# Optimization experiments

Measured on AMD Instinct MI355X. Metric: run time of the kernel, lower is better.

Reference implementation:

```python
import jax, jax.numpy as jnp
import numpy as np

B, C, H, W = 8, 256, 128, 128
HEADS = 4
HEAD_DIM = C // HEADS  # 64
SCALE = HEAD_DIM ** -0.5


def setup_inputs() -> dict:
    key = jax.random.key(0)
    k1, k2, k3 = jax.random.split(key, 3)
    x = jax.random.normal(k1, (B, C, H, W), dtype=jnp.float32)
    # 1x1 convs == per-pixel linear layers; kaiming-ish small init
    Wqkv = jax.random.normal(k2, (3 * C, C), dtype=jnp.float32) * (1.0 / np.sqrt(C))
    bqkv = jnp.zeros((3 * C,), dtype=jnp.float32)
    Wproj = jax.random.normal(k3, (C, C), dtype=jnp.float32) * (1.0 / np.sqrt(C))
    bproj = jnp.zeros((C,), dtype=jnp.float32)
    return {"x": x, "Wqkv": Wqkv, "bqkv": bqkv, "Wproj": Wproj, "bproj": bproj}


def reference(x, Wqkv, bqkv, Wproj, bproj):
    b, c, h, w = x.shape
    hw = h * w
    xf = x.reshape(b, c, hw)  # [b, c, hw]
    # 1x1 conv QKV projection
    qkv = jnp.einsum('bcn,oc->bon', xf, Wqkv) + bqkv[None, :, None]  # [b, 3c, hw]
    qkv = qkv.reshape(b, 3, HEADS, HEAD_DIM, hw)
    q, k, v = qkv[:, 0], qkv[:, 1], qkv[:, 2]  # each [b, heads, d, hw]
    # channel attention: [b, heads, d, d]
    attn = jnp.einsum('bhdn,bhen->bhde', q, k) * SCALE
    attn = jax.nn.softmax(attn, axis=-1)
    out = jnp.einsum('bhde,bhen->bhdn', attn, v).reshape(b, c, hw)
    # output 1x1 conv
    out = jnp.einsum('bcn,oc->bon', out, Wproj) + bproj[None, :, None]
    return out.reshape(b, c, h, w)
```

## Files before the change

kernel.cpp:

```cpp
#include <hip/hip_runtime.h>
#include <hip/hip_bf16.h>
#include <stdint.h>


#define HW 16384
#define SCALE_F 0.125f
#define NF 16384.0f

typedef __attribute__((ext_vector_type(8))) short bf16x8;
typedef __attribute__((ext_vector_type(4))) float f32x4;

__device__ __forceinline__ unsigned short f2bf(float f) {
    union { float f; uint32_t u; } v; v.f = f;
    uint32_t u = v.u;
    return (unsigned short)((u + 0x7fffu + ((u >> 16) & 1u)) >> 16);
}
__device__ __forceinline__ float bf2f(unsigned short s) {
    union { uint32_t u; float f; } v; v.u = ((uint32_t)s) << 16;
    return v.f;
}

__global__ __launch_bounds__(512) void gram(
        const float* __restrict__ x, float* __restrict__ partG,
        float* __restrict__ parts_s) {
    const int kc = blockIdx.x;
    const int b  = blockIdx.y;
    __shared__ __align__(16) unsigned short Hs[2][256 * 32];
    __shared__ __align__(16) unsigned short Ls[2][256 * 32];
    const int tid = threadIdx.x, lane = tid & 63, w = tid >> 6;
    const int l15 = lane & 15, lg = lane >> 4;
    const int wr = w >> 1, wc = w & 1;
    const int srow = tid >> 1, shalf = tid & 1;
    const int m4 = (srow >> 1) & 3;
    const float* xb = x + (size_t)b * 256 * HW + (size_t)srow * HW + kc * 512 + shalf * 16;
    f32x4 acc[4][8] = {};
    float rs = 0.f;
    float4 ld[4];

#define LOADR(kstep)                                                            \
    {                                                                           \
        const float4* src = reinterpret_cast<const float4*>(xb + (kstep) * 32); \
        ld[0] = src[0]; ld[1] = src[1]; ld[2] = src[2]; ld[3] = src[3];         \
    }
#define STORE(sel)                                                              \
    {                                                                           \
        _Pragma("unroll")                                                       \
        for (int cq = 0; cq < 2; ++cq) {                                        \
            union { unsigned short u[8]; uint4 v; } Hu, Lu;                     \
            const float vv[8] = {ld[2*cq].x, ld[2*cq].y, ld[2*cq].z, ld[2*cq].w,\
                                 ld[2*cq+1].x, ld[2*cq+1].y, ld[2*cq+1].z, ld[2*cq+1].w}; \
            _Pragma("unroll")                                                   \
            for (int i = 0; i < 8; ++i) {                                       \
                Hu.u[i] = f2bf(vv[i]);                                          \
                Lu.u[i] = f2bf(vv[i] - bf2f(Hu.u[i]));                          \
                rs += vv[i];                                                    \
            }                                                                   \
            const int slot = ((shalf * 2 + cq) ^ m4) << 4;                      \
            *reinterpret_cast<uint4*>((char*)(&Hs[sel][0]) + srow * 64 + slot) = Hu.v; \
            *reinterpret_cast<uint4*>((char*)(&Ls[sel][0]) + srow * 64 + slot) = Lu.v; \
        }                                                                       \
    }
#define DO_MFMA(sel)                                                            \
    {                                                                           \
        bf16x8 fah[4], fal[4];                                                  \
        _Pragma("unroll")                                                       \
        for (int i = 0; i < 4; ++i) {                                           \
            const int row = wr * 64 + i * 16 + l15;                             \
            const int off = row * 64 + ((lg ^ ((row >> 1) & 3)) << 4);          \
            fah[i] = *reinterpret_cast<const bf16x8*>((const char*)&Hs[sel][0] + off); \
            fal[i] = *reinterpret_cast<const bf16x8*>((const char*)&Ls[sel][0] + off); \
        }                                                                       \
        _Pragma("unroll")                                                       \
        for (int j = 0; j < 8; ++j) {                                           \
            const int row = wc * 128 + j * 16 + l15;                            \
            const int off = row * 64 + ((lg ^ ((row >> 1) & 3)) << 4);          \
            const bf16x8 fbh = *reinterpret_cast<const bf16x8*>((const char*)&Hs[sel][0] + off); \
            const bf16x8 fbl = *reinterpret_cast<const bf16x8*>((const char*)&Ls[sel][0] + off); \
            _Pragma("unroll")                                                   \
            for (int i = 0; i < 4; ++i) {                                       \
                acc[i][j] = __builtin_amdgcn_mfma_f32_16x16x32_bf16(fah[i], fbh, acc[i][j], 0, 0, 0); \
                acc[i][j] = __builtin_amdgcn_mfma_f32_16x16x32_bf16(fah[i], fbl, acc[i][j], 0, 0, 0); \
                acc[i][j] = __builtin_amdgcn_mfma_f32_16x16x32_bf16(fal[i], fbh, acc[i][j], 0, 0, 0); \
            }                                                                   \
        }                                                                       \
    }

    LOADR(0);
    STORE(0);
    __syncthreads();
    for (int t = 0; t < 16; ++t) {
        if (t < 15) LOADR(t + 1);
        DO_MFMA(t & 1);
        if (t < 15) STORE((t + 1) & 1);
        __syncthreads();
    }
#undef LOADR
#undef STORE
#undef DO_MFMA

    rs += __shfl_xor(rs, 1);
    if ((tid & 1) == 0) parts_s[(size_t)(b * 32 + kc) * 256 + srow] = rs;

    float* pw = partG + (size_t)(b * 32 + kc) * 65536;
    #pragma unroll
    for (int i = 0; i < 4; ++i)
        #pragma unroll
        for (int rr = 0; rr < 4; ++rr) {
            const int m = wr * 64 + i * 16 + lg * 4 + rr;
            #pragma unroll
            for (int j = 0; j < 8; ++j)
                pw[m * 256 + wc * 128 + j * 16 + l15] = acc[i][j][rr];
        }
}

__global__ __launch_bounds__(256) void greduce(
        const float* __restrict__ partG, float* __restrict__ G) {
    const size_t idx = (size_t)blockIdx.x * 256 + threadIdx.x;
    const int b = (int)(idx >> 16);
    const int i = (int)(idx & 65535);
    float sacc = 0.f;
    #pragma unroll
    for (int kc = 0; kc < 32; ++kc)
        sacc += partG[(size_t)(b * 32 + kc) * 65536 + i];
    G[idx] = sacc;
}

__global__ void sreduce(const float* __restrict__ parts_s, float* __restrict__ s) {
    const int b = blockIdx.x, c = threadIdx.x;
    float a = 0.f;
    #pragma unroll
    for (int kc = 0; kc < 32; ++kc)
        a += parts_s[(size_t)(b * 32 + kc) * 256 + c];
    s[b * 256 + c] = a;
}

__global__ __launch_bounds__(256) void tgemm(
        const float* __restrict__ G, const float* __restrict__ Wqkv,
        float* __restrict__ T) {
    const int c0 = blockIdx.x * 64;
    const int d0 = blockIdx.y * 64;
    const int b  = blockIdx.z;
    __shared__ float Ws[64][68];
    __shared__ float Gs[64][68];
    const int tid = threadIdx.x;
    const float* Gb = G + (size_t)b * 65536;
    const int ry = (tid >> 4) * 4, cx = (tid & 15) * 4;
    const int r = tid >> 2, q = (tid & 3) * 16;
    float acc[4][4] = {};

    for (int cb = 0; cb < 4; ++cb) {
        __syncthreads();
        #pragma unroll
        for (int j = 0; j < 16; j += 4) {
            *reinterpret_cast<float4*>(&Ws[r][q + j]) =
                *reinterpret_cast<const float4*>(Wqkv + (size_t)(d0 + r) * 256 + cb * 64 + q + j);
            *reinterpret_cast<float4*>(&Gs[r][q + j]) =
                *reinterpret_cast<const float4*>(Gb + (size_t)(cb * 64 + r) * 256 + c0 + q + j);
        }
        __syncthreads();
        #pragma unroll 8
        for (int k = 0; k < 64; ++k) {
            const float4 g4 = *reinterpret_cast<const float4*>(&Gs[k][cx]);
            #pragma unroll
            for (int i = 0; i < 4; ++i) {
                const float a = Ws[ry + i][k];
                acc[i][0] += a * g4.x;
                acc[i][1] += a * g4.y;
                acc[i][2] += a * g4.z;
                acc[i][3] += a * g4.w;
            }
        }
    }
    float* Tb = T + (size_t)b * 65536;
    #pragma unroll
    for (int i = 0; i < 4; ++i)
        #pragma unroll
        for (int j = 0; j < 4; ++j)
            Tb[(size_t)(d0 + ry + i) * 256 + c0 + cx + j] = acc[i][j];
}

__global__ __launch_bounds__(256) void logits_sm(
        const float* __restrict__ T, const float* __restrict__ Wqkv,
        const float* __restrict__ bqkv, const float* __restrict__ s,
        float* __restrict__ attn) {
    const int bh = blockIdx.x, b = bh >> 2, h = bh & 3;
    const int tid = threadIdx.x;
    __shared__ float Ts[64][257];
    __shared__ float Wks[64][257];
    __shared__ float lgs[64][65];
    __shared__ float qs[64], ks[64];
    const float* Tb = T + (size_t)b * 65536 + (size_t)(h * 64) * 256;
    const float* Wq = Wqkv + (size_t)(h * 64) * 256;
    const float* Wk = Wqkv + (size_t)(256 + h * 64) * 256;

    {
        const int r = tid >> 2, q = (tid & 3) * 64;
        #pragma unroll
        for (int j = 0; j < 64; j += 4) {
            const float4 t4 = *reinterpret_cast<const float4*>(Tb + (size_t)r * 256 + q + j);
            Ts[r][q + j + 0] = t4.x; Ts[r][q + j + 1] = t4.y;
            Ts[r][q + j + 2] = t4.z; Ts[r][q + j + 3] = t4.w;
            const float4 w4 = *reinterpret_cast<const float4*>(Wk + (size_t)r * 256 + q + j);
            Wks[r][q + j + 0] = w4.x; Wks[r][q + j + 1] = w4.y;
            Wks[r][q + j + 2] = w4.z; Wks[r][q + j + 3] = w4.w;
        }
    }
    if (tid < 128) {
        const int d = tid & 63;
        const float* wr = (tid < 64) ? (Wq + (size_t)d * 256) : (Wk + (size_t)d * 256);
        const float* sb = s + b * 256;
        float a = 0.f;
        for (int c = 0; c < 256; ++c) a += wr[c] * sb[c];
        if (tid < 64) qs[d] = a; else ks[d] = a;
    }
    __syncthreads();

    const int d4 = (tid >> 4) * 4, e4 = (tid & 15) * 4;
    float acc[4][4] = {};
    #pragma unroll 4
    for (int c = 0; c < 256; ++c) {
        float tv[4], wv[4];
        #pragma unroll
        for (int i = 0; i < 4; ++i) tv[i] = Ts[d4 + i][c];
        #pragma unroll
        for (int j = 0; j < 4; ++j) wv[j] = Wks[e4 + j][c];
        #pragma unroll
        for (int i = 0; i < 4; ++i)
            #pragma unroll
            for (int j = 0; j < 4; ++j)
                acc[i][j] += tv[i] * wv[j];
    }
    const float* bq = bqkv + h * 64;
    const float* bk = bqkv + 256 + h * 64;
    #pragma unroll
    for (int i = 0; i < 4; ++i) {
        const float bqi = bq[d4 + i], qsi = qs[d4 + i];
        #pragma unroll
        for (int j = 0; j < 4; ++j) {
            const int e = e4 + j;
            lgs[d4 + i][e] = SCALE_F * (acc[i][j] + bqi * ks[e] + bk[e] * qsi + NF * bqi * bk[e]);
        }
    }
    __syncthreads();
    if (tid < 64) {
        float m = -1e30f;
        for (int e = 0; e < 64; ++e) m = fmaxf(m, lgs[tid][e]);
        float sum = 0.f;
        for (int e = 0; e < 64; ++e) {
            const float ex = __expf(lgs[tid][e] - m);
            sum += ex;
            lgs[tid][e] = ex;
        }
        const float inv = 1.f / sum;
        float* ar = attn + ((size_t)bh * 64 + tid) * 64;
        for (int e = 0; e < 64; ++e) ar[e] = lgs[tid][e] * inv;
    }
}

__global__ __launch_bounds__(256) void build_M(
        const float* __restrict__ attn, const float* __restrict__ Wproj,
        float* __restrict__ M) {
    const int g = blockIdx.x * 256 + threadIdx.x;
    const int b = g >> 16, o = (g >> 8) & 255, cpx = g & 255;
    const int h = cpx >> 6, e = cpx & 63;
    const float* wrow = Wproj + (size_t)o * 256 + h * 64;
    const float* acol = attn + ((size_t)(b * 4 + h) * 64) * 64 + e;
    float sacc = 0.f;
    #pragma unroll
    for (int d = 0; d < 64; ++d) sacc += wrow[d] * acol[d * 64];
    M[g] = sacc;
}

__global__ __launch_bounds__(256) void build_P(
        const float* __restrict__ M, const float* __restrict__ Wqkv,
        const float* __restrict__ bqkv, const float* __restrict__ bproj,
        unsigned short* __restrict__ P, float* __restrict__ cvec) {
    const int b = blockIdx.x >> 4, oc = blockIdx.x & 15;
    const int tid = threadIdx.x, c = tid;
    __shared__ float Wvs[32 * 256];
    __shared__ float Ms[16 * 256];
    for (int j = tid; j < 16 * 256; j += 256)
        Ms[j] = M[(size_t)b * 65536 + oc * 16 * 256 + j];
    float acc[16];
    #pragma unroll
    for (int o = 0; o < 16; ++o) acc[o] = 0.f;
    for (int cb2 = 0; cb2 < 8; ++cb2) {
        __syncthreads();
        for (int j = tid; j < 32 * 256; j += 256)
            Wvs[j] = Wqkv[(size_t)(512 + cb2 * 32) * 256 + j];
        __syncthreads();
        for (int c2 = 0; c2 < 32; ++c2) {
            const float wv = Wvs[c2 * 256 + c];
            #pragma unroll
            for (int o = 0; o < 16; ++o)
                acc[o] += Ms[o * 256 + cb2 * 32 + c2] * wv;
        }
    }
    #pragma unroll
    for (int o = 0; o < 16; ++o)
        P[(size_t)b * 65536 + (size_t)(oc * 16 + o) * 256 + c] = f2bf(acc[o]);
    if (tid < 16) {
        const int o = oc * 16 + tid;
        float a = bproj[o];
        for (int c2 = 0; c2 < 256; ++c2)
            a += M[(size_t)b * 65536 + (size_t)o * 256 + c2] * bqkv[512 + c2];
        cvec[b * 256 + o] = a;
    }
}

__global__ __launch_bounds__(512) void out_gemm(
        const unsigned short* __restrict__ P, const float* __restrict__ x,
        const float* __restrict__ cvec, float* __restrict__ out) {
    const int n0 = blockIdx.x * 128;
    const int b  = blockIdx.y;
    __shared__ __align__(16) unsigned short Bs[8 * 128 * 32];
    const int tid = threadIdx.x, lane = tid & 63, w = tid >> 6;
    const int wr = w >> 1, wc = w & 1;
    const int l15 = lane & 15, lg = lane >> 4;
    const unsigned short* Pb = P + (size_t)b * 65536;

    {
        const int sn = tid & 127;
        const int sg = tid >> 7;
        const int wslot = ((sg ^ ((sn >> 1) & 3)) << 4);
        const float* xcol = x + (size_t)b * 256 * HW + n0 + sn;
        float bv[2][8];
        #pragma unroll
        for (int i = 0; i < 8; ++i)
            bv[0][i] = xcol[(size_t)(sg * 8 + i) * HW];
        #pragma unroll
        for (int s = 0; s < 8; ++s) {
            if (s < 7) {
                #pragma unroll
                for (int i = 0; i < 8; ++i)
                    bv[(s + 1) & 1][i] = xcol[(size_t)((s + 1) * 32 + sg * 8 + i) * HW];
            }
            union { unsigned short u[8]; uint4 v; } Bu;
            #pragma unroll
            for (int i = 0; i < 8; ++i) Bu.u[i] = f2bf(bv[s & 1][i]);
            *reinterpret_cast<uint4*>((char*)Bs + s * 8192 + sn * 64 + wslot) = Bu.v;
        }
    }
    __syncthreads();

    f32x4 acc[4][4] = {};
    const int m4r = (l15 >> 1) & 3;
    #pragma unroll
    for (int s = 0; s < 8; ++s) {
        bf16x8 fp[4];
        #pragma unroll
        for (int i = 0; i < 4; ++i)
            fp[i] = *reinterpret_cast<const bf16x8*>(
                Pb + (size_t)(wr * 64 + i * 16 + l15) * 256 + s * 32 + lg * 8);
        #pragma unroll
        for (int j = 0; j < 4; ++j) {
            const int row = wc * 64 + j * 16 + l15;
            const bf16x8 fx = *reinterpret_cast<const bf16x8*>(
                (const char*)Bs + s * 8192 + row * 64 + ((lg ^ m4r) << 4));
            #pragma unroll
            for (int i = 0; i < 4; ++i)
                acc[i][j] = __builtin_amdgcn_mfma_f32_16x16x32_bf16(fx, fp[i], acc[i][j], 0, 0, 0);
        }
    }

    float* ob = out + (size_t)b * 256 * HW;
    #pragma unroll
    for (int i = 0; i < 4; ++i) {
        const int m = wr * 64 + i * 16 + l15;
        const float bp = cvec[b * 256 + m];
        #pragma unroll
        for (int j = 0; j < 4; ++j) {
            const int n = n0 + wc * 64 + j * 16 + lg * 4;
            float4 o4;
            o4.x = acc[i][j][0] + bp;
            o4.y = acc[i][j][1] + bp;
            o4.z = acc[i][j][2] + bp;
            o4.w = acc[i][j][3] + bp;
            *reinterpret_cast<float4*>(ob + (size_t)m * HW + n) = o4;
        }
    }
}

extern "C" void kernel_launch(void* const* d_in, const int* in_sizes, int n_in,
                              void* d_out, int out_size, void* d_ws, size_t ws_size,
                              hipStream_t stream) {
    const float* x     = (const float*)d_in[0];
    const float* Wqkv  = (const float*)d_in[1];
    const float* bqkv  = (const float*)d_in[2];
    const float* Wproj = (const float*)d_in[3];
    const float* bproj = (const float*)d_in[4];
    float* out = (float*)d_out;

    char* ws = (char*)d_ws;
    float* partG   = (float*)(ws);
    float* G       = (float*)(ws + 67108864);
    float* attn    = (float*)(ws + 69206016);
    float* M       = (float*)(ws + 69730304);
    unsigned short* P = (unsigned short*)(ws + 71827456);
    float* cvec    = (float*)(ws + 72876032);
    float* s       = (float*)(ws + 72884224);
    float* parts_s = (float*)(ws + 72892416);
    float* T       = (float*)(ws + 73154560);

    gram     <<<dim3(32, 8),   512, 0, stream>>>(x, partG, parts_s);
    greduce  <<<2048,          256, 0, stream>>>(partG, G);
    sreduce  <<<8,             256, 0, stream>>>(parts_s, s);
    tgemm    <<<dim3(4, 4, 8), 256, 0, stream>>>(G, Wqkv, T);
    logits_sm<<<32,            256, 0, stream>>>(T, Wqkv, bqkv, s, attn);
    build_M  <<<2048,          256, 0, stream>>>(attn, Wproj, M);
    build_P  <<<128,           256, 0, stream>>>(M, Wqkv, bqkv, bproj, P, cvec);
    out_gemm <<<dim3(128, 8),  512, 0, stream>>>(P, x, cvec, out);
}
```

Before: 227.1 us.

## Fuse small attention-stage kernels and deepen gram load prefetch

The kernel chain drops from eight launches to five. sreduce, tgemm and logits_sm are fused into one tlogits kernel that works out the per-channel sums, the q/k bias terms and the T=WqG product in shared memory. build_M and build_P are merged into buildMP, so the M matrix is no longer written to and read back from global memory. greduce now uses float4 loads, and the gram kernel double-buffers its register loads two steps ahead. The fused kernels run on few blocks (32 and 128), which may limit parallelism, and they use large shared-memory footprints.

Result: faster. 214.3 us (-5.6%).

```diff
diff --git a/kernel.cpp b/kernel.cpp
--- a/kernel.cpp
+++ b/kernel.cpp
@@ -35,20 +35,20 @@
     const float* xb = x + (size_t)b * 256 * HW + (size_t)srow * HW + kc * 512 + shalf * 16;
     f32x4 acc[4][8] = {};
     float rs = 0.f;
-    float4 ld[4];
-
-#define LOADR(kstep)                                                            \
+    float4 ld0[4], ld1[4];
+
+#define LOADR(dst, kstep)                                                       \
     {                                                                           \
         const float4* src = reinterpret_cast<const float4*>(xb + (kstep) * 32); \
-        ld[0] = src[0]; ld[1] = src[1]; ld[2] = src[2]; ld[3] = src[3];         \
-    }
-#define STORE(sel)                                                              \
+        dst[0] = src[0]; dst[1] = src[1]; dst[2] = src[2]; dst[3] = src[3];     \
+    }
+#define STORE(sel, buf)                                                         \
     {                                                                           \
         _Pragma("unroll")                                                       \
         for (int cq = 0; cq < 2; ++cq) {                                        \
             union { unsigned short u[8]; uint4 v; } Hu, Lu;                     \
-            const float vv[8] = {ld[2*cq].x, ld[2*cq].y, ld[2*cq].z, ld[2*cq].w,\
-                                 ld[2*cq+1].x, ld[2*cq+1].y, ld[2*cq+1].z, ld[2*cq+1].w}; \
+            const float vv[8] = {buf[2*cq].x, buf[2*cq].y, buf[2*cq].z, buf[2*cq].w, \
+                                 buf[2*cq+1].x, buf[2*cq+1].y, buf[2*cq+1].z, buf[2*cq+1].w}; \
             _Pragma("unroll")                                                   \
             for (int i = 0; i < 8; ++i) {                                       \
                 Hu.u[i] = f2bf(vv[i]);                                          \
@@ -85,13 +85,18 @@
         }                                                                       \
     }
 
-    LOADR(0);
-    STORE(0);
+    LOADR(ld0, 0);
+    LOADR(ld1, 1);
+    STORE(0, ld0);
     __syncthreads();
     for (int t = 0; t < 16; ++t) {
-        if (t < 15) LOADR(t + 1);
+        if (t < 14) {
+            if (t & 1) { LOADR(ld1, t + 2); } else { LOADR(ld0, t + 2); }
+        }
         DO_MFMA(t & 1);
-        if (t < 15) STORE((t + 1) & 1);
+        if (t < 15) {
+            if ((t + 1) & 1) { STORE((t + 1) & 1, ld1); } else { STORE((t + 1) & 1, ld0); }
+        }
         __syncthreads();
     }
 #undef LOADR
@@ -114,198 +119,227 @@
 }
 
 __global__ __launch_bounds__(256) void greduce(
-        const float* __restrict__ partG, float* __restrict__ G) {
-    const size_t idx = (size_t)blockIdx.x * 256 + threadIdx.x;
-    const int b = (int)(idx >> 16);
-    const int i = (int)(idx & 65535);
-    float sacc = 0.f;
-    #pragma unroll
-    for (int kc = 0; kc < 32; ++kc)
-        sacc += partG[(size_t)(b * 32 + kc) * 65536 + i];
-    G[idx] = sacc;
-}
-
-__global__ void sreduce(const float* __restrict__ parts_s, float* __restrict__ s) {
-    const int b = blockIdx.x, c = threadIdx.x;
-    float a = 0.f;
-    #pragma unroll
-    for (int kc = 0; kc < 32; ++kc)
-        a += parts_s[(size_t)(b * 32 + kc) * 256 + c];
-    s[b * 256 + c] = a;
-}
-
-__global__ __launch_bounds__(256) void tgemm(
+        const float4* __restrict__ partG4, float4* __restrict__ G4) {
+    const int g = blockIdx.x * 256 + threadIdx.x;
+    const int b = g >> 14, i4 = g & 16383;
+    float4 a = make_float4(0.f, 0.f, 0.f, 0.f);
+    #pragma unroll 8
+    for (int kc = 0; kc < 32; ++kc) {
+        const float4 v = partG4[(size_t)(b * 32 + kc) * 16384 + i4];
+        a.x += v.x; a.y += v.y; a.z += v.z; a.w += v.w;
+    }
+    G4[g] = a;
+}
+
+__global__ __launch_bounds__(512) void tlogits(
         const float* __restrict__ G, const float* __restrict__ Wqkv,
-        float* __restrict__ T) {
-    const int c0 = blockIdx.x * 64;
-    const int d0 = blockIdx.y * 64;
-    const int b  = blockIdx.z;
-    __shared__ float Ws[64][68];
-    __shared__ float Gs[64][68];
-    const int tid = threadIdx.x;
-    const float* Gb = G + (size_t)b * 65536;
-    const int ry = (tid >> 4) * 4, cx = (tid & 15) * 4;
-    const int r = tid >> 2, q = (tid & 3) * 16;
-    float acc[4][4] = {};
-
-    for (int cb = 0; cb < 4; ++cb) {
-        __syncthreads();
-        #pragma unroll
-        for (int j = 0; j < 16; j += 4) {
-            *reinterpret_cast<float4*>(&Ws[r][q + j]) =
-                *reinterpret_cast<const float4*>(Wqkv + (size_t)(d0 + r) * 256 + cb * 64 + q + j);
-            *reinterpret_cast<float4*>(&Gs[r][q + j]) =
-                *reinterpret_cast<const float4*>(Gb + (size_t)(cb * 64 + r) * 256 + c0 + q + j);
-        }
-        __syncthreads();
-        #pragma unroll 8
-        for (int k = 0; k < 64; ++k) {
-            const float4 g4 = *reinterpret_cast<const float4*>(&Gs[k][cx]);
-            #pragma unroll
-            for (int i = 0; i < 4; ++i) {
-                const float a = Ws[ry + i][k];
-                acc[i][0] += a * g4.x;
-                acc[i][1] += a * g4.y;
-                acc[i][2] += a * g4.z;
-                acc[i][3] += a * g4.w;
-            }
-        }
-    }
-    float* Tb = T + (size_t)b * 65536;
-    #pragma unroll
-    for (int i = 0; i < 4; ++i)
-        #pragma unroll
-        for (int j = 0; j < 4; ++j)
-            Tb[(size_t)(d0 + ry + i) * 256 + c0 + cx + j] = acc[i][j];
-}
-
-__global__ __launch_bounds__(256) void logits_sm(
-        const float* __restrict__ T, const float* __restrict__ Wqkv,
-        const float* __restrict__ bqkv, const float* __restrict__ s,
+        const float* __restrict__ bqkv, const float* __restrict__ parts_s,
         float* __restrict__ attn) {
     const int bh = blockIdx.x, b = bh >> 2, h = bh & 3;
     const int tid = threadIdx.x;
-    __shared__ float Ts[64][257];
-    __shared__ float Wks[64][257];
-    __shared__ float lgs[64][65];
-    __shared__ float qs[64], ks[64];
-    const float* Tb = T + (size_t)b * 65536 + (size_t)(h * 64) * 256;
+    __shared__ __align__(16) float SM[38528];
+    float* R1 = SM;
+    float* R2 = SM + 16896;
+    float* WQ = SM + 33792;
+    float* SB = SM + 38144;
+    float* QS = SM + 38400;
+    float* KS = SM + 38464;
+    const float* Gb = G + (size_t)b * 65536;
     const float* Wq = Wqkv + (size_t)(h * 64) * 256;
     const float* Wk = Wqkv + (size_t)(256 + h * 64) * 256;
 
+    if (tid < 256) {
+        float a = 0.f;
+        #pragma unroll
+        for (int kc = 0; kc < 32; ++kc)
+            a += parts_s[(size_t)(b * 32 + kc) * 256 + tid];
+        SB[tid] = a;
+    }
     {
-        const int r = tid >> 2, q = (tid & 3) * 64;
-        #pragma unroll
-        for (int j = 0; j < 64; j += 4) {
-            const float4 t4 = *reinterpret_cast<const float4*>(Tb + (size_t)r * 256 + q + j);
-            Ts[r][q + j + 0] = t4.x; Ts[r][q + j + 1] = t4.y;
-            Ts[r][q + j + 2] = t4.z; Ts[r][q + j + 3] = t4.w;
-            const float4 w4 = *reinterpret_cast<const float4*>(Wk + (size_t)r * 256 + q + j);
-            Wks[r][q + j + 0] = w4.x; Wks[r][q + j + 1] = w4.y;
-            Wks[r][q + j + 2] = w4.z; Wks[r][q + j + 3] = w4.w;
-        }
-    }
-    if (tid < 128) {
-        const int d = tid & 63;
-        const float* wr = (tid < 64) ? (Wq + (size_t)d * 256) : (Wk + (size_t)d * 256);
-        const float* sb = s + b * 256;
+        const int e = tid >> 3, cq = (tid & 7) * 32;
+        #pragma unroll
+        for (int q = 0; q < 8; ++q) {
+            const float4 w4 = *reinterpret_cast<const float4*>(Wk + (size_t)e * 256 + cq + q * 4);
+            R2[(cq + q * 4 + 0) * 66 + e] = w4.x;
+            R2[(cq + q * 4 + 1) * 66 + e] = w4.y;
+            R2[(cq + q * 4 + 2) * 66 + e] = w4.z;
+            R2[(cq + q * 4 + 3) * 66 + e] = w4.w;
+        }
+    }
+    __syncthreads();
+    if (tid < 64) {
         float a = 0.f;
-        for (int c = 0; c < 256; ++c) a += wr[c] * sb[c];
-        if (tid < 64) qs[d] = a; else ks[d] = a;
-    }
-    __syncthreads();
-
-    const int d4 = (tid >> 4) * 4, e4 = (tid & 15) * 4;
-    float acc[4][4] = {};
-    #pragma unroll 4
+        for (int c = 0; c < 256; ++c) a += R2[c * 66 + tid] * SB[c];
+        KS[tid] = a;
+    }
+
+    const int dq = tid >> 5, cb = tid & 31;
+    float tacc[4][8] = {};
+    float qacc = 0.f;
+    for (int cc = 0; cc < 4; ++cc) {
+        {
+            const int r = tid >> 3, cq = (tid & 7) * 32;
+            #pragma unroll
+            for (int q = 0; q < 8; ++q)
+                *reinterpret_cast<float4*>(&R1[r * 264 + cq + q * 4]) =
+                    *reinterpret_cast<const float4*>(Gb + (size_t)(cc * 64 + r) * 256 + cq + q * 4);
+        }
+        {
+            const int r = tid >> 3, c8 = (tid & 7) * 8;
+            *reinterpret_cast<float4*>(&WQ[r * 68 + c8]) =
+                *reinterpret_cast<const float4*>(Wq + (size_t)r * 256 + cc * 64 + c8);
+            *reinterpret_cast<float4*>(&WQ[r * 68 + c8 + 4]) =
+                *reinterpret_cast<const float4*>(Wq + (size_t)r * 256 + cc * 64 + c8 + 4);
+        }
+        __syncthreads();
+        for (int c = 0; c < 64; ++c) {
+            float wv[4];
+            #pragma unroll
+            for (int i = 0; i < 4; ++i) wv[i] = WQ[(dq * 4 + i) * 68 + c];
+            #pragma unroll
+            for (int jj = 0; jj < 8; ++jj) {
+                const float gv = R1[c * 264 + cb + 32 * jj];
+                #pragma unroll
+                for (int i = 0; i < 4; ++i) tacc[i][jj] += wv[i] * gv;
+            }
+        }
+        if (tid < 64) {
+            float a = 0.f;
+            for (int c = 0; c < 64; ++c) a += WQ[tid * 68 + c] * SB[cc * 64 + c];
+            qacc += a;
+        }
+        __syncthreads();
+    }
+    if (tid < 64) QS[tid] = qacc;
+    #pragma unroll
+    for (int i = 0; i < 4; ++i)
+        #pragma unroll
+        for (int jj = 0; jj < 8; ++jj)
+            R1[(dq * 4 + i) * 264 + cb + 32 * jj] = tacc[i][jj];
+    __syncthreads();
+
+    const int e2 = tid & 31;
+    float lacc[4][2] = {};
     for (int c = 0; c < 256; ++c) {
-        float tv[4], wv[4];
-        #pragma unroll
-        for (int i = 0; i < 4; ++i) tv[i] = Ts[d4 + i][c];
-        #pragma unroll
-        for (int j = 0; j < 4; ++j) wv[j] = Wks[e4 + j][c];
-        #pragma unroll
-        for (int i = 0; i < 4; ++i)
-            #pragma unroll
-            for (int j = 0; j < 4; ++j)
-                acc[i][j] += tv[i] * wv[j];
-    }
+        float tv[4];
+        #pragma unroll
+        for (int i = 0; i < 4; ++i) tv[i] = R1[(dq * 4 + i) * 264 + c];
+        #pragma unroll
+        for (int k = 0; k < 2; ++k) {
+            const float wv = R2[c * 66 + e2 * 2 + k];
+            #pragma unroll
+            for (int i = 0; i < 4; ++i) lacc[i][k] += tv[i] * wv;
+        }
+    }
+    float* lgs = WQ;
     const float* bq = bqkv + h * 64;
     const float* bk = bqkv + 256 + h * 64;
     #pragma unroll
     for (int i = 0; i < 4; ++i) {
-        const float bqi = bq[d4 + i], qsi = qs[d4 + i];
-        #pragma unroll
-        for (int j = 0; j < 4; ++j) {
-            const int e = e4 + j;
-            lgs[d4 + i][e] = SCALE_F * (acc[i][j] + bqi * ks[e] + bk[e] * qsi + NF * bqi * bk[e]);
+        const int d = dq * 4 + i;
+        #pragma unroll
+        for (int k = 0; k < 2; ++k) {
+            const int e = e2 * 2 + k;
+            lgs[d * 65 + e] = SCALE_F * (lacc[i][k] + bq[d] * KS[e] + bk[e] * QS[d] + NF * bq[d] * bk[e]);
         }
     }
     __syncthreads();
     if (tid < 64) {
         float m = -1e30f;
-        for (int e = 0; e < 64; ++e) m = fmaxf(m, lgs[tid][e]);
+        for (int e = 0; e < 64; ++e) m = fmaxf(m, lgs[tid * 65 + e]);
         float sum = 0.f;
         for (int e = 0; e < 64; ++e) {
-            const float ex = __expf(lgs[tid][e] - m);
+            const float ex = __expf(lgs[tid * 65 + e] - m);
             sum += ex;
-            lgs[tid][e] = ex;
+            lgs[tid * 65 + e] = ex;
         }
         const float inv = 1.f / sum;
         float* ar = attn + ((size_t)bh * 64 + tid) * 64;
-        for (int e = 0; e < 64; ++e) ar[e] = lgs[tid][e] * inv;
-    }
-}
-
-__global__ __launch_bounds__(256) void build_M(
+        for (int e = 0; e < 64; ++e) ar[e] = lgs[tid * 65 + e] * inv;
+    }
+}
+
+__global__ __launch_bounds__(256) void buildMP(
         const float* __restrict__ attn, const float* __restrict__ Wproj,
-        float* __restrict__ M) {
-    const int g = blockIdx.x * 256 + threadIdx.x;
-    const int b = g >> 16, o = (g >> 8) & 255, cpx = g & 255;
-    const int h = cpx >> 6, e = cpx & 63;
-    const float* wrow = Wproj + (size_t)o * 256 + h * 64;
-    const float* acol = attn + ((size_t)(b * 4 + h) * 64) * 64 + e;
-    float sacc = 0.f;
-    #pragma unroll
-    for (int d = 0; d < 64; ++d) sacc += wrow[d] * acol[d * 64];
-    M[g] = sacc;
-}
-
-__global__ __launch_bounds__(256) void build_P(
-        const float* __restrict__ M, const float* __restrict__ Wqkv,
-        const float* __restrict__ bqkv, const float* __restrict__ bproj,
-        unsigned short* __restrict__ P, float* __restrict__ cvec) {
-    const int b = blockIdx.x >> 4, oc = blockIdx.x & 15;
-    const int tid = threadIdx.x, c = tid;
-    __shared__ float Wvs[32 * 256];
-    __shared__ float Ms[16 * 256];
-    for (int j = tid; j < 16 * 256; j += 256)
-        Ms[j] = M[(size_t)b * 65536 + oc * 16 * 256 + j];
-    float acc[16];
-    #pragma unroll
-    for (int o = 0; o < 16; ++o) acc[o] = 0.f;
-    for (int cb2 = 0; cb2 < 8; ++cb2) {
+        const float* __restrict__ Wqkv, const float* __restrict__ bqkv,
+        const float* __restrict__ bproj, unsigned short* __restrict__ P,
+        float* __restrict__ cvec) {
+    const int blk = blockIdx.x;
+    const int b = blk >> 4, o0 = (blk & 15) * 16;
+    const int tid = threadIdx.x;
+    __shared__ __align__(16) float U[16512];
+    __shared__ __align__(16) float WpL[16 * 258];
+    __shared__ __align__(16) float ML[16 * 258];
+    const int og = tid >> 6, cb = tid & 63;
+
+    {
+        const float* ab = attn + (size_t)b * 16384;
+        #pragma unroll
+        for (int q = 0; q < 16; ++q)
+            *reinterpret_cast<float4*>(&U[tid * 64 + q * 4]) =
+                *reinterpret_cast<const float4*>(ab + tid * 64 + q * 4);
+    }
+    {
+        const int r = tid >> 4, cc = (tid & 15) * 16;
+        #pragma unroll
+        for (int q = 0; q < 4; ++q)
+            *reinterpret_cast<float4*>(&WpL[r * 258 + cc + q * 4]) =
+                *reinterpret_cast<const float4*>(Wproj + (size_t)(o0 + r) * 256 + cc + q * 4);
+    }
+    __syncthreads();
+
+    float macc[4][4] = {};
+    #pragma unroll
+    for (int j = 0; j < 4; ++j)
+        for (int d = 0; d < 64; ++d) {
+            const float a = U[j * 4096 + d * 64 + cb];
+            #pragma unroll
+            for (int i = 0; i < 4; ++i)
+                macc[i][j] += WpL[(og * 4 + i) * 258 + j * 64 + d] * a;
+        }
+    #pragma unroll
+    for (int i = 0; i < 4; ++i)
+        #pragma unroll
+        for (int j = 0; j < 4; ++j)
+            ML[(og * 4 + i) * 258 + j * 64 + cb] = macc[i][j];
+    __syncthreads();
+
+    if (tid < 16) {
+        const int o = o0 + tid;
+        float a = bproj[o];
+        for (int he = 0; he < 256; ++he) a += ML[tid * 258 + he] * bqkv[512 + he];
+        cvec[b * 256 + o] = a;
+    }
+
+    float pacc[4][4] = {};
+    for (int ch = 0; ch < 4; ++ch) {
+        {
+            const int r = tid >> 2, cc = (tid & 3) * 64;
+            #pragma unroll
+            for (int q = 0; q < 16; ++q)
+                *reinterpret_cast<float4*>(&U[r * 258 + cc + q * 4]) =
+                    *reinterpret_cast<const float4*>(Wqkv + (size_t)(512 + ch * 64 + r) * 256 + cc + q * 4);
+        }
         __syncthreads();
-        for (int j = tid; j < 32 * 256; j += 256)
-            Wvs[j] = Wqkv[(size_t)(512 + cb2 * 32) * 256 + j];
+        for (int he = 0; he < 64; ++he) {
+            float mw[4];
+            #pragma unroll
+            for (int i = 0; i < 4; ++i) mw[i] = ML[(og * 4 + i) * 258 + ch * 64 + he];
+            #pragma unroll
+            for (int j = 0; j < 4; ++j) {
+                const float wv = U[he * 258 + j * 64 + cb];
+                #pragma unroll
+                for (int i = 0; i < 4; ++i) pacc[i][j] += mw[i] * wv;
+            }
+        }
         __syncthreads();
-        for (int c2 = 0; c2 < 32; ++c2) {
-            const float wv = Wvs[c2 * 256 + c];
-            #pragma unroll
-            for (int o = 0; o < 16; ++o)
-                acc[o] += Ms[o * 256 + cb2 * 32 + c2] * wv;
-        }
-    }
-    #pragma unroll
-    for (int o = 0; o < 16; ++o)
-        P[(size_t)b * 65536 + (size_t)(oc * 16 + o) * 256 + c] = f2bf(acc[o]);
-    if (tid < 16) {
-        const int o = oc * 16 + tid;
-        float a = bproj[o];
-        for (int c2 = 0; c2 < 256; ++c2)
-            a += M[(size_t)b * 65536 + (size_t)o * 256 + c2] * bqkv[512 + c2];
-        cvec[b * 256 + o] = a;
-    }
+    }
+    unsigned short* Pb = P + (size_t)b * 65536;
+    #pragma unroll
+    for (int i = 0; i < 4; ++i)
+        #pragma unroll
+        for (int j = 0; j < 4; ++j)
+            Pb[(size_t)(o0 + og * 4 + i) * 256 + j * 64 + cb] = f2bf(pacc[i][j]);
 }
 
 __global__ __launch_bounds__(512) void out_gemm(
@@ -395,19 +429,13 @@
     float* partG   = (float*)(ws);
     float* G       = (float*)(ws + 67108864);
     float* attn    = (float*)(ws + 69206016);
-    float* M       = (float*)(ws + 69730304);
-    unsigned short* P = (unsigned short*)(ws + 71827456);
-    float* cvec    = (float*)(ws + 72876032);
-    float* s       = (float*)(ws + 72884224);
-    float* parts_s = (float*)(ws + 72892416);
-    float* T       = (float*)(ws + 73154560);
-
-    gram     <<<dim3(32, 8),   512, 0, stream>>>(x, partG, parts_s);
-    greduce  <<<2048,          256, 0, stream>>>(partG, G);
-    sreduce  <<<8,             256, 0, stream>>>(parts_s, s);
-    tgemm    <<<dim3(4, 4, 8), 256, 0, stream>>>(G, Wqkv, T);
-    logits_sm<<<32,            256, 0, stream>>>(T, Wqkv, bqkv, s, attn);
-    build_M  <<<2048,          256, 0, stream>>>(attn, Wproj, M);
-    build_P  <<<128,           256, 0, stream>>>(M, Wqkv, bqkv, bproj, P, cvec);
-    out_gemm <<<dim3(128, 8),  512, 0, stream>>>(P, x, cvec, out);
-}
+    unsigned short* P = (unsigned short*)(ws + 69730304);
+    float* cvec    = (float*)(ws + 70778880);
+    float* parts_s = (float*)(ws + 70787072);
+
+    gram    <<<dim3(32, 8),  512, 0, stream>>>(x, partG, parts_s);
+    greduce <<<512,          256, 0, stream>>>((const float4*)partG, (float4*)G);
+    tlogits <<<32,           512, 0, stream>>>(G, Wqkv, bqkv, parts_s, attn);
+    buildMP <<<128,          256, 0, stream>>>(attn, Wproj, Wqkv, bqkv, bproj, P, cvec);
+    out_gemm<<<dim3(128, 8), 512, 0, stream>>>(P, x, cvec, out);
+}
```
